# Kernel optimization log

Hardware: AMD Instinct MI355X
Metric: run time of the kernel (lower is better)

Reference implementation:

```python
import jax, jax.numpy as jnp
import numpy as np

N_NODES = 100000
N_EDGES = 1600000
IN_C = 128
OUT_C = 64
NEG_SLOPE = 0.2  # PyG GATConv default
EPS = 1e-16      # PyG softmax denominator guard


def setup_inputs() -> dict:
    key = jax.random.key(0)
    k1, k2, k3, k4, k5, k6 = jax.random.split(key, 6)
    x = jax.random.normal(k1, (N_NODES, IN_C), dtype=jnp.float32)
    edge_index = jax.random.randint(k2, (2, N_EDGES), 0, N_NODES, dtype=jnp.int64)
    # Learned params (GATConv with heads=1): linear weight, attention vectors, bias
    W = jax.random.normal(k3, (IN_C, OUT_C), dtype=jnp.float32) * (1.0 / np.sqrt(IN_C))
    a_src = jax.random.normal(k4, (OUT_C,), dtype=jnp.float32) * (1.0 / np.sqrt(OUT_C))
    a_dst = jax.random.normal(k5, (OUT_C,), dtype=jnp.float32) * (1.0 / np.sqrt(OUT_C))
    b = jax.random.normal(k6, (OUT_C,), dtype=jnp.float32) * 0.01
    return {"x": x, "edge_index": edge_index, "W": W, "a_src": a_src, "a_dst": a_dst, "b": b}


def reference(x, edge_index, W, a_src, a_dst, b):
    N = x.shape[0]
    h = x @ W  # [N, OUT_C] transformed node features
    # add self loops (PyG default add_self_loops=True)
    loops = jnp.arange(N, dtype=edge_index.dtype)
    src = jnp.concatenate([edge_index[0], loops])  # [E+N]
    dst = jnp.concatenate([edge_index[1], loops])  # [E+N]
    # attention logits per edge: leaky_relu(a_src . h_src + a_dst . h_dst)
    s_src = h @ a_src  # [N]
    s_dst = h @ a_dst  # [N]
    logits = jax.nn.leaky_relu(s_src[src] + s_dst[dst], NEG_SLOPE)  # [E+N]
    # segment softmax over incoming edges of each destination node
    seg_max = jax.ops.segment_max(logits, dst, num_segments=N)  # [N]
    e = jnp.exp(logits - seg_max[dst])
    denom = jax.ops.segment_sum(e, dst, num_segments=N)  # [N]
    coef = e / (denom[dst] + EPS)  # [E+N]
    # weighted scatter-add of source messages
    out = jax.ops.segment_sum(coef[:, None] * h[src], dst, num_segments=N) + b  # [N, OUT_C]
    return jax.nn.elu(out)
```

## Files before the change

kernel.cpp:

```cpp
#include <hip/hip_runtime.h>
#include <math.h>

#define IN_C 128
#define OUT_C 64
#define NEG_SLOPE 0.2f
#define GAT_EPS 1e-16f

#define FSH 6
#define FN 64
#define CAPB 1536
#define PACKS 20
#define CHUNK 4096
#define BINT 1024
#define NFBA 1568
#define CSTR 4

typedef unsigned int uint;
typedef unsigned short ushort;
typedef __attribute__((ext_vector_type(8))) short bf16x8;
typedef __attribute__((ext_vector_type(4))) float f32x4;

__device__ __forceinline__ ushort f2bf(float f) {
    uint u = __float_as_uint(f);
    return (ushort)((u + 0x7fffu + ((u >> 16) & 1u)) >> 16);
}

__global__ __launch_bounds__(256) void gemm_kernel(
    const float* __restrict__ x, const float* __restrict__ W,
    const float* __restrict__ a_src, const float* __restrict__ a_dst,
    ushort* __restrict__ h16, float* __restrict__ s_src, float* __restrict__ s_dst,
    int N, int* __restrict__ zero_ptr, int zero_n)
{
    __shared__ __align__(16) ushort xs[64 * 128];
    __shared__ __align__(16) ushort Wl[128 * 64];
    const int t = threadIdx.x;

    {
        int zi = blockIdx.x * 256 + t;
        if (zi < zero_n) zero_ptr[zi] = 0;
    }

    #pragma unroll
    for (int q = 0; q < 8; q++) {
        float4 wv = ((const float4*)W)[t * 8 + q];
        #pragma unroll
        for (int e = 0; e < 4; e++) {
            int L = t * 32 + q * 4 + e;
            int k = L >> 6, col = L & 63;
            int kc = k >> 5, kg = (k >> 3) & 3, j = k & 7;
            int ct = col >> 4, c16 = col & 15;
            float v = (e == 0) ? wv.x : (e == 1) ? wv.y : (e == 2) ? wv.z : wv.w;
            Wl[(((kc * 4 + ct) * 4 + kg) * 16 + c16) * 8 + j] = f2bf(v);
        }
    }
    const int row0 = blockIdx.x * 64;
    {
        int row_l = t >> 2;
        int grow = row0 + row_l;
        #pragma unroll
        for (int qq = 0; qq < 4; qq++) {
            int kq = (t & 3) * 4 + qq;
            float4 v0 = make_float4(0.f, 0.f, 0.f, 0.f);
            float4 v1 = v0;
            if (grow < N) {
                const float4* xp = (const float4*)(x + (size_t)grow * IN_C + kq * 8);
                v0 = xp[0]; v1 = xp[1];
            }
            uint4 pk;
            pk.x = (uint)f2bf(v0.x) | ((uint)f2bf(v0.y) << 16);
            pk.y = (uint)f2bf(v0.z) | ((uint)f2bf(v0.w) << 16);
            pk.z = (uint)f2bf(v1.x) | ((uint)f2bf(v1.y) << 16);
            pk.w = (uint)f2bf(v1.z) | ((uint)f2bf(v1.w) << 16);
            int slot = row_l * 16 + (kq ^ (row_l & 7));
            *(uint4*)&xs[slot * 8] = pk;
        }
    }
    __syncthreads();

    const int wv_ = t >> 6;
    const int l = t & 63;
    const int c16 = l & 15;
    const int quad = l >> 4;
    const int row_a = wv_ * 16 + c16;

    f32x4 acc[4] = {{0.f, 0.f, 0.f, 0.f}, {0.f, 0.f, 0.f, 0.f},
                    {0.f, 0.f, 0.f, 0.f}, {0.f, 0.f, 0.f, 0.f}};

    #pragma unroll
    for (int kc = 0; kc < 4; kc++) {
        int kq = kc * 4 + quad;
        bf16x8 a = *(const bf16x8*)&xs[(row_a * 16 + (kq ^ (row_a & 7))) * 8];
        #pragma unroll
        for (int ct = 0; ct < 4; ct++) {
            bf16x8 b = *(const bf16x8*)&Wl[(((kc * 4 + ct) * 4 + quad) * 16 + c16) * 8];
            acc[ct] = __builtin_amdgcn_mfma_f32_16x16x32_bf16(a, b, acc[ct], 0, 0, 0);
        }
    }

    float as4[4], ad4[4];
    #pragma unroll
    for (int ct = 0; ct < 4; ct++) {
        as4[ct] = a_src[ct * 16 + c16];
        ad4[ct] = a_dst[ct * 16 + c16];
    }
    #pragma unroll
    for (int reg = 0; reg < 4; reg++) {
        int row = row0 + wv_ * 16 + quad * 4 + reg;
        float ps = acc[0][reg] * as4[0] + acc[1][reg] * as4[1]
                 + acc[2][reg] * as4[2] + acc[3][reg] * as4[3];
        float pd = acc[0][reg] * ad4[0] + acc[1][reg] * ad4[1]
                 + acc[2][reg] * ad4[2] + acc[3][reg] * ad4[3];
        ps += __shfl_xor(ps, 1);  pd += __shfl_xor(pd, 1);
        ps += __shfl_xor(ps, 2);  pd += __shfl_xor(pd, 2);
        ps += __shfl_xor(ps, 4);  pd += __shfl_xor(pd, 4);
        ps += __shfl_xor(ps, 8);  pd += __shfl_xor(pd, 8);
        if (row < N) {
            #pragma unroll
            for (int ct = 0; ct < 4; ct++)
                h16[(size_t)row * OUT_C + ct * 16 + c16] = f2bf(acc[ct][reg]);
            if (c16 == 0) { s_src[row] = ps; s_dst[row] = pd; }
        }
    }
}

__global__ __launch_bounds__(1024) void bin3_kernel(
    const int* __restrict__ src, const int* __restrict__ dst,
    int* __restrict__ ccur, int* __restrict__ ebufB, int E)
{
    __shared__ int    hist[NFBA];
    __shared__ int    bcur[NFBA];
    __shared__ int    rbuf[CHUNK];
    __shared__ ushort rfb[CHUNK];
    const int t = threadIdx.x;
    const int e0 = blockIdx.x * CHUNK;
    int tot = E - e0; if (tot > CHUNK) tot = CHUNK;

    for (int i = t; i < NFBA; i += BINT) hist[i] = 0;
    __syncthreads();

    const int i0 = t * 4;
    if (i0 < tot) {
        if (i0 + 3 < tot) {
            int4 d4 = *(const int4*)(dst + e0 + i0);
            int4 s4 = *(const int4*)(src + e0 + i0);
            int dd_[4] = {d4.x, d4.y, d4.z, d4.w};
            int ss_[4] = {s4.x, s4.y, s4.z, s4.w};
            #pragma unroll
            for (int k = 0; k < 4; k++) {
                int fb = dd_[k] >> FSH;
                atomicAdd(&hist[fb], 1);
                rbuf[i0 + k] = ((dd_[k] & (FN - 1)) << PACKS) | ss_[k];
                rfb[i0 + k] = (ushort)fb;
            }
        } else {
            for (int k = 0; k < 4 && i0 + k < tot; k++) {
                int dd = dst[e0 + i0 + k], ss = src[e0 + i0 + k];
                int fb = dd >> FSH;
                atomicAdd(&hist[fb], 1);
                rbuf[i0 + k] = ((dd & (FN - 1)) << PACKS) | ss;
                rfb[i0 + k] = (ushort)fb;
            }
        }
    }
    __syncthreads();

    for (int fb = t; fb < NFBA; fb += BINT) {
        int v = hist[fb];
        bcur[fb] = (v > 0) ? atomicAdd(&ccur[fb * CSTR], v) : 0;
    }
    __syncthreads();

    if (i0 < tot) {
        #pragma unroll
        for (int k = 0; k < 4; k++) {
            if (i0 + k < tot) {
                int fb = rfb[i0 + k];
                int pos = atomicAdd(&bcur[fb], 1);
                if (pos < CAPB)
                    ebufB[(size_t)fb * CAPB + pos] = rbuf[i0 + k];
            }
        }
    }
}

__global__ __launch_bounds__(256) void nodeB_kernel(
    const int* __restrict__ ccurB, const int* __restrict__ ebufB,
    const float* __restrict__ s_src, const float* __restrict__ s_dst,
    const ushort* __restrict__ h16, const float* __restrict__ bias,
    float* __restrict__ out, int N)
{
    __shared__ int   csr_s[CAPB];
    __shared__ float csr_e[CAPB];
    __shared__ int lhist[FN], lofs[FN + 1], lcur[FN];

    const int b = blockIdx.x;
    const int t = threadIdx.x;
    const int node0 = b << FSH;
    const int nn = min(FN, N - node0);
    int cnt = ccurB[b * CSTR]; if (cnt > CAPB) cnt = CAPB;
    const int base = b * CAPB;

    if (t < FN) lhist[t] = 0;
    __syncthreads();
    for (int i = t; i < cnt; i += 256)
        atomicAdd(&lhist[(ebufB[base + i] >> PACKS) & (FN - 1)], 1);
    __syncthreads();
    if (t < FN) {
        int v = lhist[t];
        int incl = v;
        #pragma unroll
        for (int off = 1; off < FN; off <<= 1) {
            int u = __shfl_up(incl, off);
            if (t >= off) incl += u;
        }
        lofs[t + 1] = incl;
        lcur[t] = incl - v;
        if (t == 0) lofs[0] = 0;
    }
    __syncthreads();
    for (int i = t; i < cnt; i += 256) {
        int pk = ebufB[base + i];
        int ld = (pk >> PACKS) & (FN - 1);
        int sj = pk & ((1 << PACKS) - 1);
        int q = atomicAdd(&lcur[ld], 1);
        float lg = s_src[sj] + s_dst[node0 + ld];
        lg = (lg > 0.f) ? lg : NEG_SLOPE * lg;
        csr_s[q] = sj;
        csr_e[q] = __expf(lg);
    }
    __syncthreads();

    const int w = t >> 6;
    const int l = t & 63;
    const int h2 = l >> 5;
    const int lp = l & 31;
    const float b0 = bias[2 * lp], b1 = bias[2 * lp + 1];

    for (int nl = w; nl < nn; nl += 4) {
        const int node = node0 + nl;
        const int jb = lofs[nl], je = lofs[nl + 1];
        float acc0 = 0.f, acc1 = 0.f, ds = 0.f;
        int j = jb + h2;
        for (; j + 6 < je; j += 8) {
            int s0 = csr_s[j],     s1 = csr_s[j + 2];
            int s2 = csr_s[j + 4], s3 = csr_s[j + 6];
            float e0 = csr_e[j],     e1 = csr_e[j + 2];
            float e2 = csr_e[j + 4], e3 = csr_e[j + 6];
            uint u0 = *(const uint*)&h16[(size_t)s0 * OUT_C + 2 * lp];
            uint u1 = *(const uint*)&h16[(size_t)s1 * OUT_C + 2 * lp];
            uint u2 = *(const uint*)&h16[(size_t)s2 * OUT_C + 2 * lp];
            uint u3 = *(const uint*)&h16[(size_t)s3 * OUT_C + 2 * lp];
            ds += (e0 + e1) + (e2 + e3);
            acc0 += e0 * __uint_as_float(u0 << 16) + e1 * __uint_as_float(u1 << 16)
                  + e2 * __uint_as_float(u2 << 16) + e3 * __uint_as_float(u3 << 16);
            acc1 += e0 * __uint_as_float(u0 & 0xffff0000u) + e1 * __uint_as_float(u1 & 0xffff0000u)
                  + e2 * __uint_as_float(u2 & 0xffff0000u) + e3 * __uint_as_float(u3 & 0xffff0000u);
        }
        for (; j < je; j += 2) {
            int sj = csr_s[j];
            float e = csr_e[j];
            uint u = *(const uint*)&h16[(size_t)sj * OUT_C + 2 * lp];
            ds += e;
            acc0 += e * __uint_as_float(u << 16);
            acc1 += e * __uint_as_float(u & 0xffff0000u);
        }
        acc0 += __shfl_xor(acc0, 32);
        acc1 += __shfl_xor(acc1, 32);
        ds   += __shfl_xor(ds, 32);

        float ls = s_src[node] + s_dst[node];
        ls = (ls > 0.f) ? ls : NEG_SLOPE * ls;
        float es = __expf(ls);
        uint us = *(const uint*)&h16[(size_t)node * OUT_C + 2 * lp];
        acc0 += es * __uint_as_float(us << 16);
        acc1 += es * __uint_as_float(us & 0xffff0000u);
        ds += es;

        float inv = 1.f / (ds + GAT_EPS);
        float v0 = acc0 * inv + b0;
        float v1 = acc1 * inv + b1;
        v0 = (v0 > 0.f) ? v0 : (__expf(v0) - 1.f);
        v1 = (v1 > 0.f) ? v1 : (__expf(v1) - 1.f);
        if (l < 32) *(float2*)&out[(size_t)node * OUT_C + 2 * lp] = make_float2(v0, v1);
    }
}

extern "C" void kernel_launch(void* const* d_in, const int* in_sizes, int n_in,
                              void* d_out, int out_size, void* d_ws, size_t ws_size,
                              hipStream_t stream)
{
    const float* x     = (const float*)d_in[0];
    const int*   ei    = (const int*)d_in[1];
    const float* W     = (const float*)d_in[2];
    const float* a_src = (const float*)d_in[3];
    const float* a_dst = (const float*)d_in[4];
    const float* b     = (const float*)d_in[5];
    float* out = (float*)d_out;

    const int N = in_sizes[0] / IN_C;
    const int E = in_sizes[1] / 2;
    const int NFB = (N + FN - 1) >> FSH;
    const int GB = (N + 63) / 64;
    const int GBIN = (E + CHUNK - 1) / CHUNK;
    const int* src = ei;
    const int* dst = ei + E;

    ushort* h16    = (ushort*)d_ws;
    float* s_src_p = (float*)(h16 + (size_t)N * OUT_C);
    float* s_dst_p = s_src_p + N;
    int*   ccur    = (int*)(s_dst_p + N);
    int*   ebufB   = ccur + NFBA * CSTR;

    gemm_kernel<<<GB, 256, 0, stream>>>(x, W, a_src, a_dst, h16, s_src_p, s_dst_p,
                                        N, ccur, NFBA * CSTR);
    bin3_kernel<<<GBIN, BINT, 0, stream>>>(src, dst, ccur, ebufB, E);
    nodeB_kernel<<<NFB, 256, 0, stream>>>(ccur, ebufB, s_src_p, s_dst_p, h16, b, out, N);
}
```

Measured before the change: 188.6 us.

## Fuse edge binning with GEMM into one launch and widen aggregation loads

Edge binning and the node GEMM now run in a single kernel: the first blocks bin edges (2048-edge chunks, 256 threads, 8 edges per thread) and the rest do the GEMM, so the two independent stages overlap on the GPU. Counter zeroing moves to a separate small kernel. The aggregation kernel keeps the packed edge words in registers instead of reading them twice, and each lane now loads 4 bf16 channels (uint2) so four edges are processed per wave step. The cost is an extra launch and more register pressure and shuffles, and the unrolled register cache assumes at most 1536 edges per bin.

Result: slower. 224.8 us (+19.2%).

```diff
diff --git a/kernel.cpp b/kernel.cpp
--- a/kernel.cpp
+++ b/kernel.cpp
@@ -10,10 +10,10 @@
 #define FN 64
 #define CAPB 1536
 #define PACKS 20
-#define CHUNK 4096
-#define BINT 1024
+#define CHUNK 2048
 #define NFBA 1568
 #define CSTR 4
+#define SMEM_BYTES 32768
 
 typedef unsigned int uint;
 typedef unsigned short ushort;
@@ -25,20 +25,83 @@
     return (ushort)((u + 0x7fffu + ((u >> 16) & 1u)) >> 16);
 }
 
-__global__ __launch_bounds__(256) void gemm_kernel(
+__global__ __launch_bounds__(256) void zero_kernel(int* __restrict__ p, int n)
+{
+    int i = blockIdx.x * 256 + threadIdx.x;
+    if (i < n) p[i] = 0;
+}
+
+__global__ __launch_bounds__(256) void fusedAB_kernel(
     const float* __restrict__ x, const float* __restrict__ W,
     const float* __restrict__ a_src, const float* __restrict__ a_dst,
     ushort* __restrict__ h16, float* __restrict__ s_src, float* __restrict__ s_dst,
-    int N, int* __restrict__ zero_ptr, int zero_n)
+    int N, const int* __restrict__ src, const int* __restrict__ dst,
+    int* __restrict__ ccur, int* __restrict__ ebufB, int E, int gbin)
 {
-    __shared__ __align__(16) ushort xs[64 * 128];
-    __shared__ __align__(16) ushort Wl[128 * 64];
+    __shared__ __align__(16) char smem[SMEM_BYTES];
     const int t = threadIdx.x;
 
-    {
-        int zi = blockIdx.x * 256 + t;
-        if (zi < zero_n) zero_ptr[zi] = 0;
-    }
+    if ((int)blockIdx.x < gbin) {
+        int*    hist = (int*)smem;
+        int*    bcur = (int*)(smem + 6272);
+        int*    rbuf = (int*)(smem + 12544);
+        ushort* rfb  = (ushort*)(smem + 20736);
+        const int e0 = blockIdx.x * CHUNK;
+        int tot = E - e0; if (tot > CHUNK) tot = CHUNK;
+
+        for (int i = t; i < NFBA; i += 256) hist[i] = 0;
+        __syncthreads();
+
+        const int i0 = t * 8;
+        if (i0 < tot) {
+            if (i0 + 7 < tot) {
+                int4 da = *(const int4*)(dst + e0 + i0);
+                int4 db = *(const int4*)(dst + e0 + i0 + 4);
+                int4 sa = *(const int4*)(src + e0 + i0);
+                int4 sb = *(const int4*)(src + e0 + i0 + 4);
+                int dd_[8] = {da.x, da.y, da.z, da.w, db.x, db.y, db.z, db.w};
+                int ss_[8] = {sa.x, sa.y, sa.z, sa.w, sb.x, sb.y, sb.z, sb.w};
+                #pragma unroll
+                for (int k = 0; k < 8; k++) {
+                    int fb = dd_[k] >> FSH;
+                    atomicAdd(&hist[fb], 1);
+                    rbuf[i0 + k] = ((dd_[k] & (FN - 1)) << PACKS) | ss_[k];
+                    rfb[i0 + k] = (ushort)fb;
+                }
+            } else {
+                for (int k = 0; k < 8 && i0 + k < tot; k++) {
+                    int dd = dst[e0 + i0 + k], ss = src[e0 + i0 + k];
+                    int fb = dd >> FSH;
+                    atomicAdd(&hist[fb], 1);
+                    rbuf[i0 + k] = ((dd & (FN - 1)) << PACKS) | ss;
+                    rfb[i0 + k] = (ushort)fb;
+                }
+            }
+        }
+        __syncthreads();
+
+        for (int fb = t; fb < NFBA; fb += 256) {
+            int v = hist[fb];
+            bcur[fb] = (v > 0) ? atomicAdd(&ccur[fb * CSTR], v) : 0;
+        }
+        __syncthreads();
+
+        if (i0 < tot) {
+            #pragma unroll
+            for (int k = 0; k < 8; k++) {
+                if (i0 + k < tot) {
+                    int fb = rfb[i0 + k];
+                    int pos = atomicAdd(&bcur[fb], 1);
+                    if (pos < CAPB)
+                        ebufB[(size_t)fb * CAPB + pos] = rbuf[i0 + k];
+                }
+            }
+        }
+        return;
+    }
+
+    ushort* xs = (ushort*)smem;
+    ushort* Wl = (ushort*)(smem + 16384);
 
     #pragma unroll
     for (int q = 0; q < 8; q++) {
@@ -53,7 +116,7 @@
             Wl[(((kc * 4 + ct) * 4 + kg) * 16 + c16) * 8 + j] = f2bf(v);
         }
     }
-    const int row0 = blockIdx.x * 64;
+    const int row0 = (blockIdx.x - gbin) * 64;
     {
         int row_l = t >> 2;
         int grow = row0 + row_l;
@@ -123,67 +186,7 @@
     }
 }
 
-__global__ __launch_bounds__(1024) void bin3_kernel(
-    const int* __restrict__ src, const int* __restrict__ dst,
-    int* __restrict__ ccur, int* __restrict__ ebufB, int E)
-{
-    __shared__ int    hist[NFBA];
-    __shared__ int    bcur[NFBA];
-    __shared__ int    rbuf[CHUNK];
-    __shared__ ushort rfb[CHUNK];
-    const int t = threadIdx.x;
-    const int e0 = blockIdx.x * CHUNK;
-    int tot = E - e0; if (tot > CHUNK) tot = CHUNK;
-
-    for (int i = t; i < NFBA; i += BINT) hist[i] = 0;
-    __syncthreads();
-
-    const int i0 = t * 4;
-    if (i0 < tot) {
-        if (i0 + 3 < tot) {
-            int4 d4 = *(const int4*)(dst + e0 + i0);
-            int4 s4 = *(const int4*)(src + e0 + i0);
-            int dd_[4] = {d4.x, d4.y, d4.z, d4.w};
-            int ss_[4] = {s4.x, s4.y, s4.z, s4.w};
-            #pragma unroll
-            for (int k = 0; k < 4; k++) {
-                int fb = dd_[k] >> FSH;
-                atomicAdd(&hist[fb], 1);
-                rbuf[i0 + k] = ((dd_[k] & (FN - 1)) << PACKS) | ss_[k];
-                rfb[i0 + k] = (ushort)fb;
-            }
-        } else {
-            for (int k = 0; k < 4 && i0 + k < tot; k++) {
-                int dd = dst[e0 + i0 + k], ss = src[e0 + i0 + k];
-                int fb = dd >> FSH;
-                atomicAdd(&hist[fb], 1);
-                rbuf[i0 + k] = ((dd & (FN - 1)) << PACKS) | ss;
-                rfb[i0 + k] = (ushort)fb;
-            }
-        }
-    }
-    __syncthreads();
-
-    for (int fb = t; fb < NFBA; fb += BINT) {
-        int v = hist[fb];
-        bcur[fb] = (v > 0) ? atomicAdd(&ccur[fb * CSTR], v) : 0;
-    }
-    __syncthreads();
-
-    if (i0 < tot) {
-        #pragma unroll
-        for (int k = 0; k < 4; k++) {
-            if (i0 + k < tot) {
-                int fb = rfb[i0 + k];
-                int pos = atomicAdd(&bcur[fb], 1);
-                if (pos < CAPB)
-                    ebufB[(size_t)fb * CAPB + pos] = rbuf[i0 + k];
-            }
-        }
-    }
-}
-
-__global__ __launch_bounds__(256) void nodeB_kernel(
+__global__ __launch_bounds__(256) void nodeC_kernel(
     const int* __restrict__ ccurB, const int* __restrict__ ebufB,
     const float* __restrict__ s_src, const float* __restrict__ s_dst,
     const ushort* __restrict__ h16, const float* __restrict__ bias,
@@ -202,8 +205,17 @@
 
     if (t < FN) lhist[t] = 0;
     __syncthreads();
-    for (int i = t; i < cnt; i += 256)
-        atomicAdd(&lhist[(ebufB[base + i] >> PACKS) & (FN - 1)], 1);
+
+    int pkr[6];
+    #pragma unroll
+    for (int r = 0; r < 6; r++) {
+        int i = t + r * 256;
+        if (i < cnt) {
+            int pk = ebufB[base + i];
+            pkr[r] = pk;
+            atomicAdd(&lhist[(pk >> PACKS) & (FN - 1)], 1);
+        }
+    }
     __syncthreads();
     if (t < FN) {
         int v = lhist[t];
@@ -218,70 +230,89 @@
         if (t == 0) lofs[0] = 0;
     }
     __syncthreads();
-    for (int i = t; i < cnt; i += 256) {
-        int pk = ebufB[base + i];
-        int ld = (pk >> PACKS) & (FN - 1);
-        int sj = pk & ((1 << PACKS) - 1);
-        int q = atomicAdd(&lcur[ld], 1);
-        float lg = s_src[sj] + s_dst[node0 + ld];
-        lg = (lg > 0.f) ? lg : NEG_SLOPE * lg;
-        csr_s[q] = sj;
-        csr_e[q] = __expf(lg);
+    #pragma unroll
+    for (int r = 0; r < 6; r++) {
+        int i = t + r * 256;
+        if (i < cnt) {
+            int pk = pkr[r];
+            int ld = (pk >> PACKS) & (FN - 1);
+            int sj = pk & ((1 << PACKS) - 1);
+            int q = atomicAdd(&lcur[ld], 1);
+            float lg = s_src[sj] + s_dst[node0 + ld];
+            lg = (lg > 0.f) ? lg : NEG_SLOPE * lg;
+            csr_s[q] = sj;
+            csr_e[q] = __expf(lg);
+        }
     }
     __syncthreads();
 
     const int w = t >> 6;
     const int l = t & 63;
-    const int h2 = l >> 5;
-    const int lp = l & 31;
-    const float b0 = bias[2 * lp], b1 = bias[2 * lp + 1];
+    const int sub = l >> 4;
+    const int ch4 = l & 15;
+    const float4 b4 = *(const float4*)&bias[4 * ch4];
 
     for (int nl = w; nl < nn; nl += 4) {
         const int node = node0 + nl;
         const int jb = lofs[nl], je = lofs[nl + 1];
-        float acc0 = 0.f, acc1 = 0.f, ds = 0.f;
-        int j = jb + h2;
-        for (; j + 6 < je; j += 8) {
-            int s0 = csr_s[j],     s1 = csr_s[j + 2];
-            int s2 = csr_s[j + 4], s3 = csr_s[j + 6];
-            float e0 = csr_e[j],     e1 = csr_e[j + 2];
-            float e2 = csr_e[j + 4], e3 = csr_e[j + 6];
-            uint u0 = *(const uint*)&h16[(size_t)s0 * OUT_C + 2 * lp];
-            uint u1 = *(const uint*)&h16[(size_t)s1 * OUT_C + 2 * lp];
-            uint u2 = *(const uint*)&h16[(size_t)s2 * OUT_C + 2 * lp];
-            uint u3 = *(const uint*)&h16[(size_t)s3 * OUT_C + 2 * lp];
+        float a0 = 0.f, a1 = 0.f, a2 = 0.f, a3 = 0.f, ds = 0.f;
+        int j = jb + sub;
+        for (; j + 12 < je; j += 16) {
+            int s0 = csr_s[j],      s1 = csr_s[j + 4];
+            int s2 = csr_s[j + 8],  s3 = csr_s[j + 12];
+            float e0 = csr_e[j],     e1 = csr_e[j + 4];
+            float e2 = csr_e[j + 8], e3 = csr_e[j + 12];
+            uint2 u0 = *(const uint2*)&h16[(size_t)s0 * OUT_C + 4 * ch4];
+            uint2 u1 = *(const uint2*)&h16[(size_t)s1 * OUT_C + 4 * ch4];
+            uint2 u2 = *(const uint2*)&h16[(size_t)s2 * OUT_C + 4 * ch4];
+            uint2 u3 = *(const uint2*)&h16[(size_t)s3 * OUT_C + 4 * ch4];
             ds += (e0 + e1) + (e2 + e3);
-            acc0 += e0 * __uint_as_float(u0 << 16) + e1 * __uint_as_float(u1 << 16)
-                  + e2 * __uint_as_float(u2 << 16) + e3 * __uint_as_float(u3 << 16);
-            acc1 += e0 * __uint_as_float(u0 & 0xffff0000u) + e1 * __uint_as_float(u1 & 0xffff0000u)
-                  + e2 * __uint_as_float(u2 & 0xffff0000u) + e3 * __uint_as_float(u3 & 0xffff0000u);
-        }
-        for (; j < je; j += 2) {
+            a0 += e0 * __uint_as_float(u0.x << 16) + e1 * __uint_as_float(u1.x << 16)
+                + e2 * __uint_as_float(u2.x << 16) + e3 * __uint_as_float(u3.x << 16);
+            a1 += e0 * __uint_as_float(u0.x & 0xffff0000u) + e1 * __uint_as_float(u1.x & 0xffff0000u)
+                + e2 * __uint_as_float(u2.x & 0xffff0000u) + e3 * __uint_as_float(u3.x & 0xffff0000u);
+            a2 += e0 * __uint_as_float(u0.y << 16) + e1 * __uint_as_float(u1.y << 16)
+                + e2 * __uint_as_float(u2.y << 16) + e3 * __uint_as_float(u3.y << 16);
+            a3 += e0 * __uint_as_float(u0.y & 0xffff0000u) + e1 * __uint_as_float(u1.y & 0xffff0000u)
+                + e2 * __uint_as_float(u2.y & 0xffff0000u) + e3 * __uint_as_float(u3.y & 0xffff0000u);
+        }
+        for (; j < je; j += 4) {
             int sj = csr_s[j];
             float e = csr_e[j];
-            uint u = *(const uint*)&h16[(size_t)sj * OUT_C + 2 * lp];
+            uint2 u = *(const uint2*)&h16[(size_t)sj * OUT_C + 4 * ch4];
             ds += e;
-            acc0 += e * __uint_as_float(u << 16);
-            acc1 += e * __uint_as_float(u & 0xffff0000u);
-        }
-        acc0 += __shfl_xor(acc0, 32);
-        acc1 += __shfl_xor(acc1, 32);
-        ds   += __shfl_xor(ds, 32);
+            a0 += e * __uint_as_float(u.x << 16);
+            a1 += e * __uint_as_float(u.x & 0xffff0000u);
+            a2 += e * __uint_as_float(u.y << 16);
+            a3 += e * __uint_as_float(u.y & 0xffff0000u);
+        }
+        a0 += __shfl_xor(a0, 16);  a0 += __shfl_xor(a0, 32);
+        a1 += __shfl_xor(a1, 16);  a1 += __shfl_xor(a1, 32);
+        a2 += __shfl_xor(a2, 16);  a2 += __shfl_xor(a2, 32);
+        a3 += __shfl_xor(a3, 16);  a3 += __shfl_xor(a3, 32);
+        ds += __shfl_xor(ds, 16);  ds += __shfl_xor(ds, 32);
 
         float ls = s_src[node] + s_dst[node];
         ls = (ls > 0.f) ? ls : NEG_SLOPE * ls;
         float es = __expf(ls);
-        uint us = *(const uint*)&h16[(size_t)node * OUT_C + 2 * lp];
-        acc0 += es * __uint_as_float(us << 16);
-        acc1 += es * __uint_as_float(us & 0xffff0000u);
+        uint2 us = *(const uint2*)&h16[(size_t)node * OUT_C + 4 * ch4];
+        a0 += es * __uint_as_float(us.x << 16);
+        a1 += es * __uint_as_float(us.x & 0xffff0000u);
+        a2 += es * __uint_as_float(us.y << 16);
+        a3 += es * __uint_as_float(us.y & 0xffff0000u);
         ds += es;
 
         float inv = 1.f / (ds + GAT_EPS);
-        float v0 = acc0 * inv + b0;
-        float v1 = acc1 * inv + b1;
+        float v0 = a0 * inv + b4.x;
+        float v1 = a1 * inv + b4.y;
+        float v2 = a2 * inv + b4.z;
+        float v3 = a3 * inv + b4.w;
         v0 = (v0 > 0.f) ? v0 : (__expf(v0) - 1.f);
         v1 = (v1 > 0.f) ? v1 : (__expf(v1) - 1.f);
-        if (l < 32) *(float2*)&out[(size_t)node * OUT_C + 2 * lp] = make_float2(v0, v1);
+        v2 = (v2 > 0.f) ? v2 : (__expf(v2) - 1.f);
+        v3 = (v3 > 0.f) ? v3 : (__expf(v3) - 1.f);
+        if (l < 16)
+            *(float4*)&out[(size_t)node * OUT_C + 4 * ch4] = make_float4(v0, v1, v2, v3);
     }
 }
 
@@ -302,6 +333,7 @@
     const int NFB = (N + FN - 1) >> FSH;
     const int GB = (N + 63) / 64;
     const int GBIN = (E + CHUNK - 1) / CHUNK;
+    const int NZ = NFBA * CSTR;
     const int* src = ei;
     const int* dst = ei + E;
 
@@ -309,10 +341,11 @@
     float* s_src_p = (float*)(h16 + (size_t)N * OUT_C);
     float* s_dst_p = s_src_p + N;
     int*   ccur    = (int*)(s_dst_p + N);
-    int*   ebufB   = ccur + NFBA * CSTR;
-
-    gemm_kernel<<<GB, 256, 0, stream>>>(x, W, a_src, a_dst, h16, s_src_p, s_dst_p,
-                                        N, ccur, NFBA * CSTR);
-    bin3_kernel<<<GBIN, BINT, 0, stream>>>(src, dst, ccur, ebufB, E);
-    nodeB_kernel<<<NFB, 256, 0, stream>>>(ccur, ebufB, s_src_p, s_dst_p, h16, b, out, N);
-}
+    int*   ebufB   = ccur + NZ;
+
+    zero_kernel<<<(NZ + 255) / 256, 256, 0, stream>>>(ccur, NZ);
+    fusedAB_kernel<<<GBIN + GB, 256, 0, stream>>>(x, W, a_src, a_dst, h16,
+                                                  s_src_p, s_dst_p, N,
+                                                  src, dst, ccur, ebufB, E, GBIN);
+    nodeC_kernel<<<NFB, 256, 0, stream>>>(ccur, ebufB, s_src_p, s_dst_p, h16, b, out, N);
+}
```
